# Kernel optimization log

Hardware: AMD Instinct MI355X
Metric: run time of the kernel (lower is better)

## Reference

```python
import jax, jax.numpy as jnp
import numpy as np

N_NODES = 50000
N_EDGES = 800000
NODE_DIM = 128
HIDDEN = 128
N_LAYERS = 2
EPS = 1e-5


def _layer_norm(h, gamma, beta):
    mu = jnp.mean(h, axis=-1, keepdims=True)
    var = jnp.mean(jnp.square(h - mu), axis=-1, keepdims=True)
    return (h - mu) * jax.lax.rsqrt(var + EPS) * gamma + beta


def setup_inputs() -> dict:
    key = jax.random.key(0)
    ks = jax.random.split(key, 12)
    s = 0.05  # small init scale for numerical sanity
    x = jax.random.normal(ks[0], (N_NODES, NODE_DIM), jnp.float32)
    edge_index = jax.random.randint(ks[1], (2, N_EDGES), 0, N_NODES, dtype=jnp.int64)
    # node_encoder: Linear(node_dim -> hidden)
    W_enc = jax.random.normal(ks[2], (HIDDEN, NODE_DIM), jnp.float32) * s
    b_enc = jnp.zeros((HIDDEN,), jnp.float32)
    # per-layer params, stacked over layers (L leading dim)
    Wm1 = jax.random.normal(ks[3], (N_LAYERS, HIDDEN, 2 * HIDDEN), jnp.float32) * s
    bm1 = jnp.zeros((N_LAYERS, HIDDEN), jnp.float32)
    Wm2 = jax.random.normal(ks[4], (N_LAYERS, HIDDEN, HIDDEN), jnp.float32) * s
    bm2 = jnp.zeros((N_LAYERS, HIDDEN), jnp.float32)
    Wu = jax.random.normal(ks[5], (N_LAYERS, HIDDEN, 2 * HIDDEN), jnp.float32) * s
    bu = jnp.zeros((N_LAYERS, HIDDEN), jnp.float32)
    gamma = jnp.ones((N_LAYERS, HIDDEN), jnp.float32)
    beta = jnp.zeros((N_LAYERS, HIDDEN), jnp.float32)
    # output_proj: Linear(hidden -> hidden)
    W_out = jax.random.normal(ks[6], (HIDDEN, HIDDEN), jnp.float32) * s
    b_out = jnp.zeros((HIDDEN,), jnp.float32)
    return {
        "x": x, "edge_index": edge_index,
        "W_enc": W_enc, "b_enc": b_enc,
        "Wm1": Wm1, "bm1": bm1, "Wm2": Wm2, "bm2": bm2,
        "Wu": Wu, "bu": bu, "gamma": gamma, "beta": beta,
        "W_out": W_out, "b_out": b_out,
    }


def reference(x, edge_index, W_enc, b_enc, Wm1, bm1, Wm2, bm2, Wu, bu, gamma, beta, W_out, b_out):
    row, col = edge_index[0], edge_index[1]
    h = x @ W_enc.T + b_enc  # [N, H]
    for l in range(N_LAYERS):
        # gather -> concat -> message MLP  ([E, 2H] -> [E, H])
        m = jnp.concatenate([h[row], h[col]], axis=-1)
        m = jax.nn.relu(m @ Wm1[l].T + bm1[l])
        m = m @ Wm2[l].T + bm2[l]
        # scatter_add over destination nodes (col)
        agg = jax.ops.segment_sum(m, col, num_segments=N_NODES)  # [N, H]
        upd = jnp.concatenate([h, agg], axis=-1) @ Wu[l].T + bu[l]
        h = _layer_norm(h + upd, gamma[l], beta[l])
    return h @ W_out.T + b_out  # node_embeddings [N, H]
```

## Files before the change

kernel.cpp:

```cpp
#include <hip/hip_runtime.h>

#define N_NODES 50000
#define N_EDGES 800000
#define HID 128
#define EPS 1e-5f
#define NBKT 782
#define ESLICE 6250

typedef __attribute__((ext_vector_type(8))) short s16x8;
typedef __attribute__((ext_vector_type(4))) float f32x4;
typedef __attribute__((ext_vector_type(4))) int i32x4;

__device__ __forceinline__ unsigned short f2bf(float f) {
  unsigned int u = __float_as_uint(f);
  u += 0x7fffu + ((u >> 16) & 1u);
  return (unsigned short)(u >> 16);
}
__device__ __forceinline__ unsigned int pack2(float a, float b) {
  return (unsigned int)f2bf(a) | ((unsigned int)f2bf(b) << 16);
}
__device__ __forceinline__ float bflo(unsigned int u) { return __uint_as_float(u << 16); }
__device__ __forceinline__ float bfhi(unsigned int u) { return __uint_as_float(u & 0xffff0000u); }
__device__ __forceinline__ float bf2f(unsigned short u) { return __uint_as_float((unsigned int)u << 16); }

__global__ __launch_bounds__(256) void prep_hist_kernel(
    const float* __restrict__ W_enc, const float* __restrict__ W_out,
    const float* __restrict__ Wm1, const float* __restrict__ Wu,
    const float* __restrict__ Wm2, const float* __restrict__ bm2,
    unsigned int* __restrict__ Wenc_b, unsigned int* __restrict__ Wout_b,
    unsigned int* __restrict__ Wpq_b, unsigned short* __restrict__ Wcat_b,
    float* __restrict__ bfold, const int* __restrict__ ei, int* __restrict__ bcounts) {
  __shared__ int lhist[NBKT];
  const int b = blockIdx.x, t = threadIdx.x;
  if (b >= 449) {
    const int e0 = (b - 449) * ESLICE;
    for (int i = t; i < NBKT; i += 256) lhist[i] = 0;
    __syncthreads();
    for (int e = e0 + t; e < e0 + ESLICE; e += 256)
      atomicAdd(&lhist[ei[N_EDGES + e] >> 6], 1);
    __syncthreads();
    for (int i = t; i < NBKT; i += 256)
      if (lhist[i]) atomicAdd(&bcounts[i], lhist[i]);
    return;
  }
  if (b < 32) {
    int i = b * 256 + t;
    Wenc_b[i] = pack2(W_enc[2 * i], W_enc[2 * i + 1]);
  } else if (b < 64) {
    int i = (b - 32) * 256 + t;
    Wout_b[i] = pack2(W_out[2 * i], W_out[2 * i + 1]);
  } else if (b < 192) {
    int i = (b - 64) * 256 + t;
    int k2 = i & 63;
    int c = (i >> 6) & 255;
    int l = i >> 14;
    const float* srow = Wm1 + ((size_t)l * 128 + (c & 127)) * 256 + ((c >> 7) << 7);
    Wpq_b[i] = pack2(srow[2 * k2], srow[2 * k2 + 1]);
  } else if (b < 448) {
    int i = (b - 192) * 256 + t;
    int k = i & 255, c = (i >> 8) & 127, l = i >> 15;
    const float* wrow = Wu + ((size_t)l * 128 + c) * 256;
    float v;
    if (k < 128) {
      v = wrow[k];
    } else {
      const float* wb = wrow + 128;
      const float* m2 = Wm2 + (size_t)l * 128 * 128 + (k - 128);
      float s = 0.f;
      for (int j = 0; j < 128; ++j) s += wb[j] * m2[(size_t)j * 128];
      v = s;
    }
    Wcat_b[i] = f2bf(v);
  } else {
    int l = t >> 7, c = t & 127;
    const float* wb = Wu + ((size_t)l * 128 + c) * 256 + 128;
    const float* bv = bm2 + l * 128;
    float s = 0.f;
    for (int j = 0; j < 128; ++j) s += wb[j] * bv[j];
    bfold[t] = s;
  }
}

__global__ __launch_bounds__(1024) void bscan_kernel(const int* __restrict__ bcounts,
                                                     int* __restrict__ boff,
                                                     int* __restrict__ bcursor) {
  __shared__ int wtot[16];
  const int t = threadIdx.x, lane = t & 63, w = t >> 6;
  int v = (t < NBKT) ? bcounts[t] : 0;
  int s = v;
#pragma unroll
  for (int off = 1; off < 64; off <<= 1) {
    int tt = __shfl_up(s, off);
    if (lane >= off) s += tt;
  }
  if (lane == 63) wtot[w] = s;
  __syncthreads();
  int woff = 0;
#pragma unroll
  for (int j = 0; j < 16; ++j) { int tv = wtot[j]; if (j < w) woff += tv; }
  int excl = woff + (s - v);
  if (t < NBKT) { boff[t] = excl; bcursor[t] = excl; }
  if (t == NBKT) boff[NBKT] = excl;
}

__global__ __launch_bounds__(256) void bscatter_kernel(const int* __restrict__ ei,
                                                       int* __restrict__ bcursor,
                                                       unsigned int* __restrict__ ebuf) {
  __shared__ int lhist[784];
  __shared__ int lstart[784];
  __shared__ int lcur[784];
  __shared__ int gbase[784];
  __shared__ unsigned int staged[ESLICE];
  __shared__ int wtot[4];
  const int t = threadIdx.x, lane = t & 63, w = t >> 6;
  const int e0 = blockIdx.x * ESLICE;

  for (int i = t; i < 784; i += 256) lhist[i] = 0;
  __syncthreads();
  for (int e = e0 + t; e < e0 + ESLICE; e += 256)
    atomicAdd(&lhist[ei[N_EDGES + e] >> 6], 1);
  __syncthreads();

  int tsum = 0;
  if (t < 196) tsum = lhist[4 * t] + lhist[4 * t + 1] + lhist[4 * t + 2] + lhist[4 * t + 3];
  int inc = tsum;
#pragma unroll
  for (int off = 1; off < 64; off <<= 1) {
    int tt = __shfl_up(inc, off);
    if (lane >= off) inc += tt;
  }
  if (lane == 63) wtot[w] = inc;
  __syncthreads();
  int woff = 0;
#pragma unroll
  for (int j = 0; j < 4; ++j) { int tv = wtot[j]; if (j < w) woff += tv; }
  if (t < 196) {
    int run = woff + inc - tsum;
#pragma unroll
    for (int j = 0; j < 4; ++j) {
      lstart[4 * t + j] = run;
      lcur[4 * t + j] = run;
      run += lhist[4 * t + j];
    }
  }
  for (int bk = t; bk < NBKT; bk += 256)
    gbase[bk] = lhist[bk] ? atomicAdd(&bcursor[bk], lhist[bk]) : 0;
  __syncthreads();

  for (int e = e0 + t; e < e0 + ESLICE; e += 256) {
    int s = ei[e], d = ei[N_EDGES + e];
    int pos = atomicAdd(&lcur[d >> 6], 1);
    staged[pos] = (unsigned int)s | ((unsigned int)(d & 63) << 16);
  }
  __syncthreads();

  for (int bk = w; bk < NBKT; bk += 4) {
    int cnt = lhist[bk];
    if (!cnt) continue;
    int gb = gbase[bk], ls = lstart[bk];
    for (int i = lane; i < cnt; i += 64) ebuf[gb + i] = staged[ls + i];
  }
}

__global__ __launch_bounds__(256) void sort64_kernel(const unsigned int* __restrict__ ebuf,
                                                     const int* __restrict__ boff,
                                                     unsigned int* __restrict__ esrc,
                                                     int* __restrict__ noff,
                                                     int* __restrict__ counts) {
  __shared__ int hist[64];
  __shared__ int lcur[64];
  const int b = blockIdx.x, t = threadIdx.x;
  const int e0 = boff[b], e1 = boff[b + 1];
  if (t < 64) hist[t] = 0;
  __syncthreads();
  for (int e = e0 + t; e < e1; e += 256)
    atomicAdd(&hist[(ebuf[e] >> 16) & 63], 1);
  __syncthreads();
  if (t < 64) {
    int v = hist[t];
    int s = v;
#pragma unroll
    for (int off = 1; off < 64; off <<= 1) {
      int tt = __shfl_up(s, off);
      if (t >= off) s += tt;
    }
    lcur[t] = s - v;
    int node = b * 64 + t;
    if (node < N_NODES) {
      noff[node] = e0 + s - v;
      counts[node] = v;
    }
  }
  __syncthreads();
  for (int e = e0 + t; e < e1; e += 256) {
    unsigned int pk = ebuf[e];
    int pos = atomicAdd(&lcur[(pk >> 16) & 63], 1);
    esrc[e0 + pos] = pk & 0xffffu;
  }
  if (b == NBKT - 1 && t == 0) noff[N_NODES] = e1;
}

__global__ __launch_bounds__(256) void aggregate3_kernel(
    const unsigned int* __restrict__ pq32, const float* __restrict__ bm1,
    const int* __restrict__ noff, const unsigned int* __restrict__ esrc,
    unsigned int* __restrict__ rb32) {
  const int node = blockIdx.x * 8 + (threadIdx.x >> 5);
  const int l = threadIdx.x & 31;
  uint2 qv = *(const uint2*)(pq32 + (size_t)node * 128 + 64 + 2 * l);
  float4 bv = *(const float4*)(bm1 + 4 * l);
  float q0 = bflo(qv.x) + bv.x, q1 = bfhi(qv.x) + bv.y;
  float q2 = bflo(qv.y) + bv.z, q3 = bfhi(qv.y) + bv.w;
  float a0 = 0.f, a1 = 0.f, a2 = 0.f, a3 = 0.f;
  const int i1 = noff[node + 1];
  int idx = noff[node];
  for (; idx + 3 < i1; idx += 4) {
    int s0 = esrc[idx], s1 = esrc[idx + 1], s2 = esrc[idx + 2], s3 = esrc[idx + 3];
    uint2 u0 = *(const uint2*)(pq32 + (size_t)s0 * 128 + 2 * l);
    uint2 u1 = *(const uint2*)(pq32 + (size_t)s1 * 128 + 2 * l);
    uint2 u2 = *(const uint2*)(pq32 + (size_t)s2 * 128 + 2 * l);
    uint2 u3 = *(const uint2*)(pq32 + (size_t)s3 * 128 + 2 * l);
    a0 += fmaxf(bflo(u0.x) + q0, 0.f) + fmaxf(bflo(u1.x) + q0, 0.f) +
          fmaxf(bflo(u2.x) + q0, 0.f) + fmaxf(bflo(u3.x) + q0, 0.f);
    a1 += fmaxf(bfhi(u0.x) + q1, 0.f) + fmaxf(bfhi(u1.x) + q1, 0.f) +
          fmaxf(bfhi(u2.x) + q1, 0.f) + fmaxf(bfhi(u3.x) + q1, 0.f);
    a2 += fmaxf(bflo(u0.y) + q2, 0.f) + fmaxf(bflo(u1.y) + q2, 0.f) +
          fmaxf(bflo(u2.y) + q2, 0.f) + fmaxf(bflo(u3.y) + q2, 0.f);
    a3 += fmaxf(bfhi(u0.y) + q3, 0.f) + fmaxf(bfhi(u1.y) + q3, 0.f) +
          fmaxf(bfhi(u2.y) + q3, 0.f) + fmaxf(bfhi(u3.y) + q3, 0.f);
  }
  for (; idx < i1; ++idx) {
    uint2 u0 = *(const uint2*)(pq32 + (size_t)esrc[idx] * 128 + 2 * l);
    a0 += fmaxf(bflo(u0.x) + q0, 0.f);
    a1 += fmaxf(bfhi(u0.x) + q1, 0.f);
    a2 += fmaxf(bflo(u0.y) + q2, 0.f);
    a3 += fmaxf(bfhi(u0.y) + q3, 0.f);
  }
  uint2 r;
  r.x = pack2(a0, a1);
  r.y = pack2(a2, a3);
  *(uint2*)(rb32 + (size_t)node * 64 + 2 * l) = r;
}

template <int KS, bool AF32, bool DUAL, int MODE>
__global__ __launch_bounds__(256, DUAL ? 1 : 2) void gemm3(
    const void* __restrict__ A0v, const unsigned short* __restrict__ A1,
    const unsigned short* __restrict__ W, const float* __restrict__ bias,
    const int* __restrict__ deg, const float* __restrict__ bias2,
    const float* __restrict__ gamma, const float* __restrict__ beta,
    const unsigned short* __restrict__ hres, float* __restrict__ outF,
    unsigned short* __restrict__ outB, int outw) {
  constexpr int KW = KS * 32;
  constexpr int NFRAG = KS * 8;
  __shared__ short Bs[NFRAG * 512];
  const int lane = threadIdx.x & 63;
  const int w = threadIdx.x >> 6;
  const int cl = lane & 15;
  const int kb = (lane >> 4) * 8;
  const int co = blockIdx.y * 128;
  W += (size_t)blockIdx.y * 128 * KW;

  for (int f = w; f < NFRAG; f += 4) {
    int nt = f & 7, ks = f >> 3;
    s16x8 bv = *(const s16x8*)(W + (size_t)(nt * 16 + cl) * KW + ks * 32 + kb);
    *(s16x8*)(Bs + f * 512 + lane * 8) = bv;
  }
  __syncthreads();

  s16x8 breg[KS][8];
#pragma unroll
  for (int ks = 0; ks < KS; ++ks)
#pragma unroll
    for (int nt = 0; nt < 8; ++nt)
      breg[ks][nt] = *(const s16x8*)(Bs + (ks * 8 + nt) * 512 + lane * 8);

  float bs[8], b2[8], gs[8], bes[8];
#pragma unroll
  for (int nt = 0; nt < 8; ++nt) {
    int col = nt * 16 + cl;
    bs[nt] = bias ? bias[col] : 0.f;
    if constexpr (MODE == 2) {
      b2[nt] = bias2[col];
      gs[nt] = gamma[col];
      bes[nt] = beta[col];
    }
  }

  const int step = gridDim.x * 4;
  for (int rt = blockIdx.x * 4 + w; rt < 3125; rt += step) {
    const int arow = rt * 16 + cl;
    f32x4 acc[8];
#pragma unroll
    for (int i = 0; i < 8; ++i) acc[i] = (f32x4){0.f, 0.f, 0.f, 0.f};
#pragma unroll
    for (int ks = 0; ks < KS; ++ks) {
      s16x8 a;
      if constexpr (AF32) {
        const float* ap = (const float*)A0v + (size_t)arow * HID + ks * 32 + kb;
        float4 lo = *(const float4*)ap;
        float4 hi = *(const float4*)(ap + 4);
        i32x4 ai = {(int)pack2(lo.x, lo.y), (int)pack2(lo.z, lo.w),
                    (int)pack2(hi.x, hi.y), (int)pack2(hi.z, hi.w)};
        a = __builtin_bit_cast(s16x8, ai);
      } else if constexpr (DUAL) {
        const unsigned short* base = (ks < KS / 2) ? (const unsigned short*)A0v : A1;
        int kss = (ks < KS / 2) ? ks : ks - KS / 2;
        a = *(const s16x8*)(base + (size_t)arow * HID + kss * 32 + kb);
      } else {
        a = *(const s16x8*)((const unsigned short*)A0v + (size_t)arow * HID + ks * 32 + kb);
      }
#pragma unroll
      for (int nt = 0; nt < 8; ++nt)
        acc[nt] = __builtin_amdgcn_mfma_f32_16x16x32_bf16(a, breg[ks][nt], acc[nt], 0, 0, 0);
    }

    const int rbase = rt * 16 + (lane >> 4) * 4;
    if constexpr (MODE == 2) {
#pragma unroll
      for (int reg = 0; reg < 4; ++reg) {
        int row = rbase + reg;
        float dv = (float)deg[row];
        float v[8];
        float s = 0.f, s2 = 0.f;
#pragma unroll
        for (int nt = 0; nt < 8; ++nt) {
          float hv = bf2f(hres[(size_t)row * HID + nt * 16 + cl]);
          v[nt] = acc[nt][reg] + bs[nt] + dv * b2[nt] + hv;
          s += v[nt];
          s2 += v[nt] * v[nt];
        }
#pragma unroll
        for (int m = 1; m < 16; m <<= 1) {
          s += __shfl_xor(s, m);
          s2 += __shfl_xor(s2, m);
        }
        float mu = s * (1.f / 128.f);
        float var = s2 * (1.f / 128.f) - mu * mu;
        float inv = rsqrtf(var + EPS);
#pragma unroll
        for (int nt = 0; nt < 8; ++nt) {
          float o = (v[nt] - mu) * inv * gs[nt] + bes[nt];
          outB[(size_t)row * HID + nt * 16 + cl] = f2bf(o);
        }
      }
    } else {
#pragma unroll
      for (int reg = 0; reg < 4; ++reg) {
        int row = rbase + reg;
#pragma unroll
        for (int nt = 0; nt < 8; ++nt) {
          float vv = acc[nt][reg] + bs[nt];
          if constexpr (MODE == 0) outF[(size_t)row * outw + co + nt * 16 + cl] = vv;
          else outB[(size_t)row * outw + co + nt * 16 + cl] = f2bf(vv);
        }
      }
    }
  }
}

extern "C" void kernel_launch(void* const* d_in, const int* in_sizes, int n_in,
                              void* d_out, int out_size, void* d_ws, size_t ws_size,
                              hipStream_t stream) {
  const float* x     = (const float*)d_in[0];
  const int*   ei    = (const int*)d_in[1];
  const float* W_enc = (const float*)d_in[2];
  const float* b_enc = (const float*)d_in[3];
  const float* Wm1   = (const float*)d_in[4];
  const float* bm1   = (const float*)d_in[5];
  const float* Wm2   = (const float*)d_in[6];
  const float* bm2   = (const float*)d_in[7];
  const float* Wu    = (const float*)d_in[8];
  const float* bu    = (const float*)d_in[9];
  const float* gamma = (const float*)d_in[10];
  const float* beta  = (const float*)d_in[11];
  const float* W_out = (const float*)d_in[12];
  const float* b_out = (const float*)d_in[13];
  float* out = (float*)d_out;

  char* ws = (char*)d_ws;
  const size_t NBH = (size_t)N_NODES * HID * 2;

  unsigned short* hb = (unsigned short*)(ws);
  unsigned short* pq = (unsigned short*)(ws + NBH);
  unsigned short* rb = (unsigned short*)(ws + 3 * NBH);
  char* wp = ws + 4 * NBH;
  unsigned short* Wenc_b = (unsigned short*)wp;
  unsigned short* Wout_b = Wenc_b + 16384;
  unsigned short* Wpq_b  = Wout_b + 16384;
  unsigned short* Wcat_b = Wpq_b + 65536;
  float*          bfold  = (float*)(Wcat_b + 65536);
  int* counts  = (int*)(bfold + 256);
  int* noff    = counts + N_NODES;
  int* boff    = noff + N_NODES + 1;
  int* bcounts = boff + NBKT + 1;
  int* bcursor = bcounts + NBKT;
  unsigned int* esrc = (unsigned int*)(bcursor + NBKT);
  unsigned int* ebuf = (unsigned int*)(ws + NBH);

  hipMemsetAsync(bcounts, 0, NBKT * sizeof(int), stream);
  prep_hist_kernel<<<449 + 128, 256, 0, stream>>>(
      W_enc, W_out, Wm1, Wu, Wm2, bm2, (unsigned int*)Wenc_b, (unsigned int*)Wout_b,
      (unsigned int*)Wpq_b, Wcat_b, bfold, ei, bcounts);
  bscan_kernel<<<1, 1024, 0, stream>>>(bcounts, boff, bcursor);
  bscatter_kernel<<<128, 256, 0, stream>>>(ei, bcursor, ebuf);
  sort64_kernel<<<NBKT, 256, 0, stream>>>(ebuf, boff, esrc, noff, counts);

  gemm3<4, true, false, 1><<<512, 256, 0, stream>>>(
      x, nullptr, Wenc_b, b_enc, nullptr, nullptr, nullptr, nullptr, nullptr,
      nullptr, hb, HID);

  for (int l = 0; l < 2; ++l) {
    const unsigned short* Wpql  = Wpq_b + l * 32768;
    const unsigned short* Wcatl = Wcat_b + l * 32768;
    const float* bm1l = bm1 + l * HID;
    const float* bul  = bu + l * HID;
    const float* bfl  = bfold + l * HID;
    const float* gl   = gamma + l * HID;
    const float* bl   = beta + l * HID;

    gemm3<4, false, false, 1><<<dim3(512, 2), 256, 0, stream>>>(
        hb, nullptr, Wpql, nullptr, nullptr, nullptr, nullptr, nullptr, nullptr,
        nullptr, pq, 256);
    aggregate3_kernel<<<6250, 256, 0, stream>>>((const unsigned int*)pq, bm1l, noff,
                                                esrc, (unsigned int*)rb);
    gemm3<8, false, true, 2><<<256, 256, 0, stream>>>(
        hb, rb, Wcatl, bul, counts, bfl, gl, bl, hb, nullptr, hb, HID);
  }

  gemm3<4, false, false, 0><<<512, 256, 0, stream>>>(
      hb, nullptr, Wout_b, b_out, nullptr, nullptr, nullptr, nullptr, nullptr,
      out, nullptr, HID);
}
```

Before: 253.3 us.

## Split edge aggregation across two half-waves and widen bucket scatter slices

The aggregation kernel now gives each node a full 64-lane wave. The two 32-lane halves process alternating edges and are combined with a cross-half shuffle, which doubles the memory-level parallelism per node for the gather. The bucket scatter uses twice as many slices of half the size. Each staged entry now carries its bucket id so the copy-out loop is flat and coalesced instead of per-bucket. The cost is that each thread handles fewer edges and the grid has more blocks.

```diff
diff --git a/kernel.cpp b/kernel.cpp
--- a/kernel.cpp
+++ b/kernel.cpp
@@ -5,7 +5,8 @@
 #define HID 128
 #define EPS 1e-5f
 #define NBKT 782
-#define ESLICE 6250
+#define ESLICE 3125
+#define NSLICE 256
 
 typedef __attribute__((ext_vector_type(8))) short s16x8;
 typedef __attribute__((ext_vector_type(4))) float f32x4;
@@ -150,15 +151,15 @@
   for (int e = e0 + t; e < e0 + ESLICE; e += 256) {
     int s = ei[e], d = ei[N_EDGES + e];
     int pos = atomicAdd(&lcur[d >> 6], 1);
-    staged[pos] = (unsigned int)s | ((unsigned int)(d & 63) << 16);
-  }
-  __syncthreads();
-
-  for (int bk = w; bk < NBKT; bk += 4) {
-    int cnt = lhist[bk];
-    if (!cnt) continue;
-    int gb = gbase[bk], ls = lstart[bk];
-    for (int i = lane; i < cnt; i += 64) ebuf[gb + i] = staged[ls + i];
+    staged[pos] = (unsigned int)s | ((unsigned int)(d & 63) << 16) |
+                  ((unsigned int)(d >> 6) << 22);
+  }
+  __syncthreads();
+
+  for (int i = t; i < ESLICE; i += 256) {
+    unsigned int pk = staged[i];
+    int bk = pk >> 22;
+    ebuf[gbase[bk] + (i - lstart[bk])] = pk;
   }
 }
 
@@ -200,21 +201,24 @@
   if (b == NBKT - 1 && t == 0) noff[N_NODES] = e1;
 }
 
-__global__ __launch_bounds__(256) void aggregate3_kernel(
+__global__ __launch_bounds__(256) void aggregate4_kernel(
     const unsigned int* __restrict__ pq32, const float* __restrict__ bm1,
     const int* __restrict__ noff, const unsigned int* __restrict__ esrc,
     unsigned int* __restrict__ rb32) {
-  const int node = blockIdx.x * 8 + (threadIdx.x >> 5);
-  const int l = threadIdx.x & 31;
+  const int node = blockIdx.x * 4 + (threadIdx.x >> 6);
+  const int lane = threadIdx.x & 63;
+  const int l = lane & 31;
+  const int eh = lane >> 5;
   uint2 qv = *(const uint2*)(pq32 + (size_t)node * 128 + 64 + 2 * l);
   float4 bv = *(const float4*)(bm1 + 4 * l);
   float q0 = bflo(qv.x) + bv.x, q1 = bfhi(qv.x) + bv.y;
   float q2 = bflo(qv.y) + bv.z, q3 = bfhi(qv.y) + bv.w;
   float a0 = 0.f, a1 = 0.f, a2 = 0.f, a3 = 0.f;
-  const int i1 = noff[node + 1];
-  int idx = noff[node];
-  for (; idx + 3 < i1; idx += 4) {
-    int s0 = esrc[idx], s1 = esrc[idx + 1], s2 = esrc[idx + 2], s3 = esrc[idx + 3];
+  const int i0 = noff[node], i1 = noff[node + 1];
+  const int nfull = (i1 - i0) >> 3;
+  int idx = i0 + eh;
+  for (int j = 0; j < nfull; ++j, idx += 8) {
+    int s0 = esrc[idx], s1 = esrc[idx + 2], s2 = esrc[idx + 4], s3 = esrc[idx + 6];
     uint2 u0 = *(const uint2*)(pq32 + (size_t)s0 * 128 + 2 * l);
     uint2 u1 = *(const uint2*)(pq32 + (size_t)s1 * 128 + 2 * l);
     uint2 u2 = *(const uint2*)(pq32 + (size_t)s2 * 128 + 2 * l);
@@ -228,17 +232,23 @@
     a3 += fmaxf(bfhi(u0.y) + q3, 0.f) + fmaxf(bfhi(u1.y) + q3, 0.f) +
           fmaxf(bfhi(u2.y) + q3, 0.f) + fmaxf(bfhi(u3.y) + q3, 0.f);
   }
-  for (; idx < i1; ++idx) {
+  for (; idx < i1; idx += 2) {
     uint2 u0 = *(const uint2*)(pq32 + (size_t)esrc[idx] * 128 + 2 * l);
     a0 += fmaxf(bflo(u0.x) + q0, 0.f);
     a1 += fmaxf(bfhi(u0.x) + q1, 0.f);
     a2 += fmaxf(bflo(u0.y) + q2, 0.f);
     a3 += fmaxf(bfhi(u0.y) + q3, 0.f);
   }
-  uint2 r;
-  r.x = pack2(a0, a1);
-  r.y = pack2(a2, a3);
-  *(uint2*)(rb32 + (size_t)node * 64 + 2 * l) = r;
+  a0 += __shfl_xor(a0, 32);
+  a1 += __shfl_xor(a1, 32);
+  a2 += __shfl_xor(a2, 32);
+  a3 += __shfl_xor(a3, 32);
+  if (lane < 32) {
+    uint2 r;
+    r.x = pack2(a0, a1);
+    r.y = pack2(a2, a3);
+    *(uint2*)(rb32 + (size_t)node * 64 + 2 * l) = r;
+  }
 }
 
 template <int KS, bool AF32, bool DUAL, int MODE>
@@ -397,11 +407,11 @@
   unsigned int* ebuf = (unsigned int*)(ws + NBH);
 
   hipMemsetAsync(bcounts, 0, NBKT * sizeof(int), stream);
-  prep_hist_kernel<<<449 + 128, 256, 0, stream>>>(
+  prep_hist_kernel<<<449 + NSLICE, 256, 0, stream>>>(
       W_enc, W_out, Wm1, Wu, Wm2, bm2, (unsigned int*)Wenc_b, (unsigned int*)Wout_b,
       (unsigned int*)Wpq_b, Wcat_b, bfold, ei, bcounts);
   bscan_kernel<<<1, 1024, 0, stream>>>(bcounts, boff, bcursor);
-  bscatter_kernel<<<128, 256, 0, stream>>>(ei, bcursor, ebuf);
+  bscatter_kernel<<<NSLICE, 256, 0, stream>>>(ei, bcursor, ebuf);
   sort64_kernel<<<NBKT, 256, 0, stream>>>(ebuf, boff, esrc, noff, counts);
 
   gemm3<4, true, false, 1><<<512, 256, 0, stream>>>(
@@ -420,8 +430,8 @@
     gemm3<4, false, false, 1><<<dim3(512, 2), 256, 0, stream>>>(
         hb, nullptr, Wpql, nullptr, nullptr, nullptr, nullptr, nullptr, nullptr,
         nullptr, pq, 256);
-    aggregate3_kernel<<<6250, 256, 0, stream>>>((const unsigned int*)pq, bm1l, noff,
-                                                esrc, (unsigned int*)rb);
+    aggregate4_kernel<<<12500, 256, 0, stream>>>((const unsigned int*)pq, bm1l, noff,
+                                                 esrc, (unsigned int*)rb);
     gemm3<8, false, true, 2><<<256, 256, 0, stream>>>(
         hb, rb, Wcatl, bul, counts, bfl, gl, bl, hb, nullptr, hb, HID);
   }
```

After: 222.0 us. 12.4% less time.
